# Kernel optimization log

Hardware: AMD Instinct MI355X
Metric: run time of the kernel (lower is better)

The kernel has to match this reference:

```python
import jax, jax.numpy as jnp
import numpy as np

B, IC, OC, K, H, W = 8, 512, 512, 3, 32, 32
GAIN, LRMUL = 1.0, 1.0
# compute_runtime_coef: fan_in = prod(weight_shape[:-1])
RC_CONV = GAIN / np.sqrt(K * K * IC) * LRMUL   # conv weight [K,K,IC,OC]
RC_DENSE = GAIN / np.sqrt(IC) * LRMUL          # dense weight [IC, IC]


def setup_inputs() -> dict:
    key = jax.random.key(0)
    ks = jax.random.split(key, 4)
    x = jax.random.normal(ks[0], (B, IC, H, W), dtype=jnp.float32)
    w = jax.random.normal(ks[1], (B, IC), dtype=jnp.float32)
    # init_std = 1/lrmul = 1.0 for both weights; bias init zeros
    conv_w = jax.random.normal(ks[2], (K, K, IC, OC), dtype=jnp.float32)
    dense_w = jax.random.normal(ks[3], (IC, IC), dtype=jnp.float32)
    dense_b = jnp.zeros((IC,), dtype=jnp.float32)
    return {"x": x, "w": w, "conv_w": conv_w, "dense_w": dense_w, "dense_b": dense_b}


def reference(x, w, conv_w, dense_w, dense_b):
    b, ic, h, wd = x.shape
    # modulation: style = Dense(w) + bias + 1
    style = w @ (RC_DENSE * dense_w) + LRMUL * dense_b + 1.0        # [B, IC]
    wt = (RC_CONV * conv_w)[None] * style[:, None, None, :, None]   # [B,K,K,IC,OC]
    # demodulation: rsqrt of sum of squares over (kh, kw, ic)
    d = jax.lax.rsqrt(jnp.sum(jnp.square(wt), axis=(1, 2, 3)) + 1e-8)  # [B, OC]
    wt = wt * d[:, None, None, None, :]
    # grouped conv with groups = batch: weight -> OIHW [B*OC, IC, K, K]
    w_g = jnp.transpose(wt, (0, 4, 3, 1, 2)).reshape(b * OC, ic, K, K)
    xg = x.reshape(1, b * ic, h, wd)
    y = jax.lax.conv_general_dilated(
        xg, w_g, window_strides=(1, 1), padding="SAME",
        dimension_numbers=("NCHW", "OIHW", "NCHW"), feature_group_count=b)
    return y.reshape(b, OC, h, wd)
```

## Files before the change

kernel.cpp:

```cpp
#include <hip/hip_runtime.h>
#include <stdint.h>


#define B_   8
#define IC_  512
#define OC_  512

static constexpr float RC_DENSE = 0.04419417382415922f;
static constexpr float RC_CONV  = 0.014731391274719739f;

typedef _Float16 half8    __attribute__((ext_vector_type(8)));
typedef float    floatx16 __attribute__((ext_vector_type(16)));

__device__ __forceinline__ void g2l(const void* g, void* l) {
  __builtin_amdgcn_global_load_lds(
      (const __attribute__((address_space(1))) void*)g,
      (__attribute__((address_space(3))) void*)l, 16, 0, 0);
}

__global__ __launch_bounds__(256) void style_kernel(
    const float* __restrict__ wv, const float* __restrict__ dw,
    const float* __restrict__ db, float* __restrict__ sm,
    float* __restrict__ sm2) {
  const int b = blockIdx.y;
  const int i = blockIdx.x * 64 + (threadIdx.x & 63);
  const int jg = threadIdx.x >> 6;
  __shared__ float red[4][64];
  float p = 0.f;
  for (int j = jg * 128; j < jg * 128 + 128; ++j)
    p += wv[b * IC_ + j] * dw[(size_t)j * IC_ + i];
  red[jg][threadIdx.x & 63] = p;
  __syncthreads();
  if (threadIdx.x < 64) {
    float s = red[0][threadIdx.x] + red[1][threadIdx.x] +
              red[2][threadIdx.x] + red[3][threadIdx.x];
    s = s * RC_DENSE + db[i] + 1.0f;
    float v = s * RC_CONV;
    sm[b * IC_ + i] = v;
    sm2[b * IC_ + i] = v * v;
  }
}

__global__ __launch_bounds__(256) void prep_kernel(
    const float* __restrict__ cw, const float* __restrict__ x,
    const float* __restrict__ sm, const float* __restrict__ sm2,
    _Float16* __restrict__ Wtf, float* __restrict__ dpart,
    _Float16* __restrict__ xsp) {
  __shared__ __align__(16) char smem[33280];
  const int bid = blockIdx.x;
  const int tid = threadIdx.x;
  if (bid < 256) {
    _Float16* LA = (_Float16*)smem;
    float* redall = (float*)(smem + 18432);
    const int by2 = bid >> 4, icb = bid & 15;
    const int by = by2 >> 1, h2 = by2 & 1;
    const int oc0 = by * 64 + h2 * 32, ic0 = icb * 32;
    const int ocl = tid & 31, g = tid >> 5;
    float sq4[4] = {};
    for (int m = 0; m < 36; ++m) {
      int r = m * 8 + g;
      int t = r >> 5, icl = r & 31;
      float v = cw[(size_t)(t * IC_ + ic0 + icl) * OC_ + oc0 + ocl];
      sq4[m & 3] += v * v;
      LA[m * 256 + ocl * 8 + g] = (_Float16)v;
    }
    for (int b = 0; b < 8; ++b) {
      float p = 0.f;
      for (int s = 0; s < 4; ++s)
        p += sm2[b * IC_ + ic0 + g + 8 * s] * sq4[s];
      redall[(b * 8 + g) * 32 + ocl] = p;
    }
    __syncthreads();
    _Float16* dst = Wtf + (size_t)(by * 16 + icb) * 18432;
    for (int it = 0; it < 5; ++it) {
      int c = it * 256 + tid;
      if (c < 1152) {
        int m = c >> 5, o2 = c & 31;
        *(half8*)(dst + (size_t)(m * 64 + h2 * 32 + o2) * 8) =
            *(const half8*)&LA[m * 256 + o2 * 8];
      }
    }
    const int bb = tid >> 5, o3 = tid & 31;
    float s = 0.f;
    for (int g2 = 0; g2 < 8; ++g2) s += redall[(bb * 8 + g2) * 32 + o3];
    dpart[(size_t)icb * 4096 + bb * OC_ + oc0 + o3] = s;
  } else {
    _Float16* Xt = (_Float16*)smem;
    const int rb = bid - 256;
    const int b = rb >> 5, h = rb & 31;
    for (int k = 0; k < 16; ++k) {
      int idx = k * 256 + tid;
      int ic = idx >> 3, wc = (idx & 7) * 4;
      float4 v = *(const float4*)&x[((size_t)(b * IC_ + ic) * 32 + h) * 32 + wc];
      float s = sm[b * IC_ + ic];
      Xt[(wc + 0) * 520 + ic] = (_Float16)(v.x * s);
      Xt[(wc + 1) * 520 + ic] = (_Float16)(v.y * s);
      Xt[(wc + 2) * 520 + ic] = (_Float16)(v.z * s);
      Xt[(wc + 3) * 520 + ic] = (_Float16)(v.w * s);
    }
    __syncthreads();
    _Float16* xb = xsp + (size_t)b * 16 * 36992;
    const int r = h + 1;
    half8 z = {};
    for (int it = 0; it < 9; ++it) {
      int c = it * 256 + tid;
      if (c < 2176) {
        int icb = c / 136, rem = c - 136 * icb, kkq = rem / 34, C = rem - 34 * kkq;
        half8 val = z;
        if (C != 0 && C != 33)
          val = *(const half8*)&Xt[(C - 1) * 520 + icb * 32 + kkq * 8];
        *(half8*)&xb[(size_t)icb * 36992 + (size_t)r * 1088 + kkq * 272 + C * 8] = val;
      }
    }
    if (h == 0 || h == 31) {
      const int rz = (h == 0) ? 0 : 33;
      for (int it = 0; it < 9; ++it) {
        int c = it * 256 + tid;
        if (c < 2176) {
          int icb = c / 136, rem = c - 136 * icb, kkq = rem / 34, C = rem - 34 * kkq;
          *(half8*)&xb[(size_t)icb * 36992 + (size_t)rz * 1088 + kkq * 272 + C * 8] = z;
        }
      }
    }
  }
}

__global__ __launch_bounds__(256, 2) void conv_kernel(
    const _Float16* __restrict__ Wtf,
    const _Float16* __restrict__ xsp,
    const float* __restrict__ dpart,
    float* __restrict__ out) {
  const int by = blockIdx.x, bx = blockIdx.y, b = blockIdx.z;
  const int tid = threadIdx.x, lane = tid & 63, w = tid >> 6;
  const int wm = w & 1, wn = w >> 1;
  const int n = lane & 31, kq = lane >> 5;
  const int h0 = bx * 4;

  __shared__ __align__(16) _Float16 As[2][9216];
  __shared__ __align__(16) _Float16 Xs[2][3264];
  __shared__ float redd[4][64];
  __shared__ float dvl[64];

  const _Float16* gX = xsp + (size_t)b * 16 * 36992 + (size_t)h0 * 1088;
  const _Float16* gA = Wtf + (size_t)(by * 16) * 18432;

  auto stage = [&](int st, int p) {
    const int icb = st >> 1, kk = st & 1;
    const _Float16* a = gA + (size_t)icb * 18432 + kk * 1024;
#pragma unroll
    for (int it = 0; it < 5; ++it) {
      int c = it * 256 + tid;
      if (c < 1152) {
        int r = c >> 7, o = c & 127;
        g2l(a + r * 2048 + o * 8, &As[p][c * 8]);
      }
    }
    const _Float16* xg = gX + (size_t)icb * 36992 + kk * 544;
#pragma unroll
    for (int it = 0; it < 2; ++it) {
      int c = it * 256 + tid;
      if (c < 408) {
        int r = c / 68, o = c - r * 68;
        g2l(xg + r * 1088 + o * 8, &Xs[p][c * 8]);
      }
    }
  };

  floatx16 acc[2] = {};
  stage(0, 0);
  for (int st = 0; st < 32; ++st) {
    const int cur = st & 1;
    __syncthreads();
    if (st + 1 < 32) stage(st + 1, cur ^ 1);
    const _Float16* Ap = &As[cur][0] + kq * 512 + (wm * 32 + n) * 8;
    const _Float16* Xp = &Xs[cur][0] + (wn * 2) * 544 + kq * 272 + n * 8;
    half8 a[9];
#pragma unroll
    for (int t = 0; t < 9; ++t) a[t] = *(const half8*)(Ap + t * 1024);
#pragma unroll
    for (int s = 0; s < 4; ++s) {
#pragma unroll
      for (int kw = 0; kw < 3; ++kw) {
        half8 xv = *(const half8*)(Xp + s * 544 + kw * 8);
#pragma unroll
        for (int kh = 0; kh < 3; ++kh) {
          int j = s - kh;
          if (j >= 0 && j < 2)
            acc[j] = __builtin_amdgcn_mfma_f32_32x32x16_f16(
                a[kh * 3 + kw], xv, acc[j], 0, 0, 0);
        }
      }
    }
  }

  __syncthreads();
  {
    const int oc_l = tid & 63, ig = tid >> 6;
    float s = 0.f;
    for (int k = 0; k < 4; ++k)
      s += dpart[(size_t)(ig * 4 + k) * 4096 + b * OC_ + by * 64 + oc_l];
    redd[ig][oc_l] = s;
  }
  __syncthreads();
  if (tid < 64)
    dvl[tid] = rsqrtf(redd[0][tid] + redd[1][tid] + redd[2][tid] +
                      redd[3][tid] + 1e-8f);
  __syncthreads();
  const int oc0 = by * 64 + wm * 32;
  const int r0 = h0 + wn * 2;
#pragma unroll
  for (int rg = 0; rg < 16; ++rg) {
    const int row = (rg & 3) + 8 * (rg >> 2) + 4 * kq;
    const float dv = dvl[wm * 32 + row];
    float* op = out + ((size_t)b * OC_ + oc0 + row) * 1024 + r0 * 32 + n;
    op[0]  = acc[0][rg] * dv;
    op[32] = acc[1][rg] * dv;
  }
}

extern "C" void kernel_launch(void* const* d_in, const int* in_sizes, int n_in,
                              void* d_out, int out_size, void* d_ws, size_t ws_size,
                              hipStream_t stream) {
  const float* x       = (const float*)d_in[0];
  const float* w       = (const float*)d_in[1];
  const float* conv_w  = (const float*)d_in[2];
  const float* dense_w = (const float*)d_in[3];
  const float* dense_b = (const float*)d_in[4];
  float* out = (float*)d_out;

  char* ws = (char*)d_ws;
  float*    sm    = (float*)ws;
  float*    sm2   = (float*)(ws + (16 << 10));
  float*    dpart = (float*)(ws + (32 << 10));
  _Float16* Wtf   = (_Float16*)(ws + (288 << 10));
  _Float16* xsp   = (_Float16*)(ws + (288 << 10) + 4718592);

  style_kernel<<<dim3(8, B_), 256, 0, stream>>>(w, dense_w, dense_b, sm, sm2);
  prep_kernel<<<512, 256, 0, stream>>>(conv_w, x, sm, sm2, Wtf, dpart, xsp);
  conv_kernel<<<dim3(8, 8, B_), 256, 0, stream>>>(Wtf, xsp, dpart, out);
}
```

Before: 130.2 us.

## Halve conv block output tile to 32 OC and double grid for occupancy

The conv kernel now gives each block 32 output channels instead of 64, and each wave computes one output row with a single accumulator. This doubles the grid to 1024 blocks, halves the weight LDS buffer, and raises launch bounds to 4 blocks per CU to improve occupancy and latency hiding. Staging loads are redistributed per wave. The cost is less reuse per block: each X tile is loaded twice as often, and the ratio of MFMA work to loads per block drops.

```diff
diff --git a/kernel.cpp b/kernel.cpp
--- a/kernel.cpp
+++ b/kernel.cpp
@@ -125,96 +125,92 @@
   }
 }
 
-__global__ __launch_bounds__(256, 2) void conv_kernel(
+__global__ __launch_bounds__(256, 4) void conv_kernel(
     const _Float16* __restrict__ Wtf,
     const _Float16* __restrict__ xsp,
     const float* __restrict__ dpart,
     float* __restrict__ out) {
-  const int by = blockIdx.x, bx = blockIdx.y, b = blockIdx.z;
+  const int byq = blockIdx.x & 7, hoc = blockIdx.x >> 3;
+  const int bx = blockIdx.y, b = blockIdx.z;
   const int tid = threadIdx.x, lane = tid & 63, w = tid >> 6;
-  const int wm = w & 1, wn = w >> 1;
   const int n = lane & 31, kq = lane >> 5;
   const int h0 = bx * 4;
 
-  __shared__ __align__(16) _Float16 As[2][9216];
+  __shared__ __align__(16) _Float16 As[2][4608];
   __shared__ __align__(16) _Float16 Xs[2][3264];
-  __shared__ float redd[4][64];
-  __shared__ float dvl[64];
+  __shared__ float redd[8][32];
+  __shared__ float dvl[32];
 
   const _Float16* gX = xsp + (size_t)b * 16 * 36992 + (size_t)h0 * 1088;
-  const _Float16* gA = Wtf + (size_t)(by * 16) * 18432;
+  const _Float16* gA = Wtf + (size_t)byq * 16 * 18432 + hoc * 256;
+
+  const int nA = (w == 0) ? 3 : 2;
+  const int iA = (w == 0) ? 0 : 1 + 2 * w;
 
   auto stage = [&](int st, int p) {
     const int icb = st >> 1, kk = st & 1;
     const _Float16* a = gA + (size_t)icb * 18432 + kk * 1024;
-#pragma unroll
-    for (int it = 0; it < 5; ++it) {
-      int c = it * 256 + tid;
-      if (c < 1152) {
-        int r = c >> 7, o = c & 127;
-        g2l(a + r * 2048 + o * 8, &As[p][c * 8]);
-      }
+    for (int k = 0; k < nA; ++k) {
+      int c = (iA + k) * 64 + lane;
+      int r = c >> 5, o2 = c & 31;
+      g2l(a + ((r >> 1) * 4 + (r & 1)) * 512 + o2 * 8, &As[p][c * 8]);
     }
     const _Float16* xg = gX + (size_t)icb * 36992 + kk * 544;
-#pragma unroll
-    for (int it = 0; it < 2; ++it) {
-      int c = it * 256 + tid;
-      if (c < 408) {
-        int r = c / 68, o = c - r * 68;
-        g2l(xg + r * 1088 + o * 8, &Xs[p][c * 8]);
+    {
+      int c = w * 102 + lane;
+      int r = c / 68, o = c - r * 68;
+      g2l(xg + r * 1088 + o * 8, &Xs[p][c * 8]);
+      c += 64;
+      if (lane < 38) {
+        int r2 = c / 68, o2x = c - r2 * 68;
+        g2l(xg + r2 * 1088 + o2x * 8, &Xs[p][c * 8]);
       }
     }
   };
 
-  floatx16 acc[2] = {};
+  floatx16 acc = {};
   stage(0, 0);
   for (int st = 0; st < 32; ++st) {
     const int cur = st & 1;
     __syncthreads();
     if (st + 1 < 32) stage(st + 1, cur ^ 1);
-    const _Float16* Ap = &As[cur][0] + kq * 512 + (wm * 32 + n) * 8;
-    const _Float16* Xp = &Xs[cur][0] + (wn * 2) * 544 + kq * 272 + n * 8;
+    const _Float16* Ap = &As[cur][0] + kq * 256 + n * 8;
+    const _Float16* Xp = &Xs[cur][0] + w * 544 + kq * 272 + n * 8;
     half8 a[9];
 #pragma unroll
-    for (int t = 0; t < 9; ++t) a[t] = *(const half8*)(Ap + t * 1024);
-#pragma unroll
-    for (int s = 0; s < 4; ++s) {
+    for (int t = 0; t < 9; ++t) a[t] = *(const half8*)(Ap + t * 512);
+#pragma unroll
+    for (int s = 0; s < 3; ++s) {
 #pragma unroll
       for (int kw = 0; kw < 3; ++kw) {
         half8 xv = *(const half8*)(Xp + s * 544 + kw * 8);
-#pragma unroll
-        for (int kh = 0; kh < 3; ++kh) {
-          int j = s - kh;
-          if (j >= 0 && j < 2)
-            acc[j] = __builtin_amdgcn_mfma_f32_32x32x16_f16(
-                a[kh * 3 + kw], xv, acc[j], 0, 0, 0);
-        }
-      }
-    }
-  }
-
+        acc = __builtin_amdgcn_mfma_f32_32x32x16_f16(a[s * 3 + kw], xv, acc,
+                                                     0, 0, 0);
+      }
+    }
+  }
+
+  const int oc0 = byq * 64 + hoc * 32;
   __syncthreads();
   {
-    const int oc_l = tid & 63, ig = tid >> 6;
-    float s = 0.f;
-    for (int k = 0; k < 4; ++k)
-      s += dpart[(size_t)(ig * 4 + k) * 4096 + b * OC_ + by * 64 + oc_l];
+    const int oc_l = tid & 31, ig = tid >> 5;
+    float s = dpart[(size_t)(ig * 2) * 4096 + b * OC_ + oc0 + oc_l] +
+              dpart[(size_t)(ig * 2 + 1) * 4096 + b * OC_ + oc0 + oc_l];
     redd[ig][oc_l] = s;
   }
   __syncthreads();
-  if (tid < 64)
-    dvl[tid] = rsqrtf(redd[0][tid] + redd[1][tid] + redd[2][tid] +
-                      redd[3][tid] + 1e-8f);
-  __syncthreads();
-  const int oc0 = by * 64 + wm * 32;
-  const int r0 = h0 + wn * 2;
+  if (tid < 32) {
+    float s = 1e-8f;
+#pragma unroll
+    for (int g = 0; g < 8; ++g) s += redd[g][tid];
+    dvl[tid] = rsqrtf(s);
+  }
+  __syncthreads();
 #pragma unroll
   for (int rg = 0; rg < 16; ++rg) {
     const int row = (rg & 3) + 8 * (rg >> 2) + 4 * kq;
-    const float dv = dvl[wm * 32 + row];
-    float* op = out + ((size_t)b * OC_ + oc0 + row) * 1024 + r0 * 32 + n;
-    op[0]  = acc[0][rg] * dv;
-    op[32] = acc[1][rg] * dv;
+    float* op = out + ((size_t)b * OC_ + oc0 + row) * 1024 + (h0 + w) * 32 + n;
+    op[0] = acc[rg] * dvl[row];
   }
 }
 
@@ -237,5 +233,5 @@
 
   style_kernel<<<dim3(8, B_), 256, 0, stream>>>(w, dense_w, dense_b, sm, sm2);
   prep_kernel<<<512, 256, 0, stream>>>(conv_w, x, sm, sm2, Wtf, dpart, xsp);
-  conv_kernel<<<dim3(8, 8, B_), 256, 0, stream>>>(Wtf, xsp, dpart, out);
-}
+  conv_kernel<<<dim3(16, 8, B_), 256, 0, stream>>>(Wtf, xsp, dpart, out);
+}
```

After: 135.0 us. 1.04x slower.
